# Optimization experiments

Hardware: AMD Instinct MI355X
Metric: run time of the kernel (lower is better)

## Reference

```python
import jax, jax.numpy as jnp
import numpy as np

ROI, P = 28, 7          # ROI window on feature map; output grid 7x7 -> 4x4 bins
BIN = ROI // P
C, CLASSES = 64, 2      # channels after vgg features[:2]; n classes
H = W = 512
N_ROI = 2000
D_FC = 4096


def setup_inputs() -> dict:
    key = jax.random.key(0)
    k = jax.random.split(key, 8)
    s = 0.02
    return {
        "img": jax.random.normal(k[0], (3, H, W), jnp.float32),
        "regions": jax.random.randint(k[1], (N_ROI, 2), 0, H - ROI, jnp.int32),
        "conv_w": jax.random.normal(k[2], (C, 3, 3, 3), jnp.float32) * s,
        "conv_b": jnp.zeros((C,), jnp.float32),
        "fc1_w": jax.random.normal(k[3], (D_FC, C * P * P), jnp.float32) * s,
        "fc1_b": jnp.zeros((D_FC,), jnp.float32),
        "fc2_w": jax.random.normal(k[4], (D_FC, D_FC), jnp.float32) * s,
        "fc2_b": jnp.zeros((D_FC,), jnp.float32),
        "cls_w": jax.random.normal(k[5], (CLASSES, D_FC), jnp.float32) * s,
        "cls_b": jnp.zeros((CLASSES,), jnp.float32),
        "bbox_w": jax.random.normal(k[6], (CLASSES * 4, D_FC), jnp.float32) * s,
        "bbox_b": jnp.zeros((CLASSES * 4,), jnp.float32),
    }


def reference(img, regions, conv_w, conv_b, fc1_w, fc1_b,
              fc2_w, fc2_b, cls_w, cls_b, bbox_w, bbox_b):
    # conv trunk: vgg16.features[:2] = Conv2d(3,64,3,pad=1) + ReLU
    fmap = jax.lax.conv_general_dilated(
        img[None], conv_w, window_strides=(1, 1), padding="SAME",
        dimension_numbers=("NCHW", "OIHW", "NCHW"))[0]
    fmap = jax.nn.relu(fmap + conv_b[:, None, None])        # [C, H, W]

    # per-region crop (irregular gather), vectorized over regions
    def crop(rc):
        return jax.lax.dynamic_slice(fmap, (0, rc[0], rc[1]), (C, ROI, ROI))
    rois = jax.vmap(crop)(regions)                          # [N, C, ROI, ROI]

    # RoI max pooling: divide ROIxROI window into PxP grid, max each bin
    pooled = rois.reshape(N_ROI, C, P, BIN, P, BIN).max(axis=(3, 5))  # [N,C,P,P]
    feat = pooled.reshape(N_ROI, C * P * P)

    # vgg classifier[:-1] (Dropout = identity at inference)
    feat = jax.nn.relu(feat @ fc1_w.T + fc1_b)
    feat = jax.nn.relu(feat @ fc2_w.T + fc2_b)              # [N, 4096]

    cls_logits = feat @ cls_w.T + cls_b                     # [N, CLASSES]
    loc_bbox = feat @ bbox_w.T + bbox_b                     # [N, CLASSES*4]
    return (cls_logits, loc_bbox)
```

## Files before the change

kernel.cpp:

```cpp
#include <hip/hip_runtime.h>

typedef unsigned short u16;
typedef unsigned int u32;
using bf16x8 = __attribute__((ext_vector_type(8))) short;
using f32x4  = __attribute__((ext_vector_type(4))) float;
using ushort8 = __attribute__((ext_vector_type(8))) unsigned short;

__device__ __forceinline__ u16 f2bf(float f) {
  u32 u = __float_as_uint(f);
  return (u16)((u + 0x7FFFu + ((u >> 16) & 1u)) >> 16);
}
__device__ __forceinline__ float bf2f(u16 h) {
  return __uint_as_float(((u32)h) << 16);
}
__device__ __forceinline__ ushort8 umax8(ushort8 a, ushort8 b) {
  return __builtin_elementwise_max(a, b);
}
__device__ __forceinline__ void cvt_chunk(const float* __restrict__ in,
                                          u16* __restrict__ out, int i) {
  float4 v = ((const float4*)in)[i];
  uint2 o;
  o.x = (u32)f2bf(v.x) | ((u32)f2bf(v.y) << 16);
  o.y = (u32)f2bf(v.z) | ((u32)f2bf(v.w) << 16);
  ((uint2*)out)[i] = o;
}

__global__ __launch_bounds__(512) void conv_vmax_k(
    const float* __restrict__ img, const float* __restrict__ w,
    const float* __restrict__ bias, u16* __restrict__ M1,
    const float* __restrict__ w1f, u16* __restrict__ w1b) {
  const int t = threadIdx.x;
  const int bid = blockIdx.x;
  const int r3 = bid % 3, q3 = bid / 3;
  if (r3 == 2) {
    int idx = q3 * 512 + t;
    for (int i = idx; i < 3211264; i += 262144) cvt_chunk(w1f, w1b, i);
    return;
  }
  const int widx = q3 * 2 + r3;
  const int x = ((widx & 15) << 5) + (t >> 4);
  const int cq = (t & 15) << 2;
  const int y0 = (widx >> 4) << 3;

  float wr[27][4];
#pragma unroll
  for (int p = 0; p < 27; ++p)
#pragma unroll
    for (int c = 0; c < 4; ++c) wr[p][c] = w[(cq + c) * 27 + p];
  float bz[4];
#pragma unroll
  for (int c = 0; c < 4; ++c) bz[c] = bias[cq + c];

  const bool xm = (x > 0), xp = (x < 511);
  float win[3][3][3];

#define LOADROW(yy, s)                                                        \
  do {                                                                        \
    if ((yy) >= 0 && (yy) <= 511) {                                          \
      _Pragma("unroll") for (int ci = 0; ci < 3; ++ci) {                      \
        const float* rp = img + ci * 262144 + (yy) * 512 + x;                 \
        win[ci][s][0] = xm ? rp[-1] : 0.f;                                    \
        win[ci][s][1] = rp[0];                                                \
        win[ci][s][2] = xp ? rp[1] : 0.f;                                     \
      }                                                                        \
    } else {                                                                   \
      _Pragma("unroll") for (int ci = 0; ci < 3; ++ci) {                      \
        win[ci][s][0] = 0.f; win[ci][s][1] = 0.f; win[ci][s][2] = 0.f;        \
      }                                                                        \
    }                                                                          \
  } while (0)

  LOADROW(y0 - 1, 0);
  LOADROW(y0, 1);

  float h0[4], h1[4], h2[4], cur[4];
#pragma unroll
  for (int i = 0; i < 11; ++i) {
    const int r = y0 + i;
    LOADROW(r + 1, 2);
    if (r <= 511) {
#pragma unroll
      for (int c = 0; c < 4; ++c) cur[c] = bz[c];
#pragma unroll
      for (int ci = 0; ci < 3; ++ci)
#pragma unroll
        for (int ky = 0; ky < 3; ++ky)
#pragma unroll
          for (int kx = 0; kx < 3; ++kx) {
            const float iv = win[ci][ky][kx];
            const int p = ci * 9 + ky * 3 + kx;
#pragma unroll
            for (int c = 0; c < 4; ++c) cur[c] = fmaf(wr[p][c], iv, cur[c]);
          }
#pragma unroll
      for (int c = 0; c < 4; ++c) cur[c] = fmaxf(cur[c], 0.f);
    } else {
#pragma unroll
      for (int c = 0; c < 4; ++c) cur[c] = 0.f;
    }
    if (i >= 3) {
      const int ym = r - 3;
      float m[4];
#pragma unroll
      for (int c = 0; c < 4; ++c)
        m[c] = fmaxf(fmaxf(h0[c], h1[c]), fmaxf(h2[c], cur[c]));
      uint2 o;
      o.x = (u32)f2bf(m[0]) | ((u32)f2bf(m[1]) << 16);
      o.y = (u32)f2bf(m[2]) | ((u32)f2bf(m[3]) << 16);
      *(uint2*)(M1 + (((size_t)(ym * 512 + x)) << 6) + cq) = o;
    }
#pragma unroll
    for (int c = 0; c < 4; ++c) { h0[c] = h1[c]; h1[c] = h2[c]; h2[c] = cur[c]; }
#pragma unroll
    for (int ci = 0; ci < 3; ++ci)
#pragma unroll
      for (int kx = 0; kx < 3; ++kx) {
        win[ci][0][kx] = win[ci][1][kx];
        win[ci][1][kx] = win[ci][2][kx];
      }
  }
#undef LOADROW
}

__global__ __launch_bounds__(256) void roipool2_k(
    const u16* __restrict__ M1, const int* __restrict__ regions,
    u16* __restrict__ feat, const float* __restrict__ w2f,
    u16* __restrict__ w2b) {
  const int t = threadIdx.x;
  const int bid = blockIdx.x;
  const int r5 = bid % 5, q5 = bid / 5;
  if (r5 == 4) {
    int idx = q5 * 256 + t;
    for (int i = idx; i < 4194304; i += 131072) cvt_chunk(w2f, w2b, i);
    return;
  }
  const int n = q5 * 4 + r5;
  uint4* fdst = (uint4*)(feat + (size_t)n * 3136);
  if (n >= 2000) {
    uint4 z; z.x = z.y = z.z = z.w = 0u;
    for (int w = t; w < 392; w += 256) fdst[w] = z;
    return;
  }
  __shared__ u16 frow[3136];
  int r0 = regions[2 * n], c0 = regions[2 * n + 1];
  for (int w = t; w < 392; w += 256) {
    int bin = w >> 3, cg = w & 7;
    int py = bin / 7, px = bin % 7;
    int y = r0 + py * 4, xb = c0 + px * 4;
    const u16* base = M1 + (((size_t)(y * 512 + xb)) << 6) + cg * 8;
    ushort8 a = *(const ushort8*)(base);
    ushort8 b = *(const ushort8*)(base + 64);
    ushort8 c = *(const ushort8*)(base + 128);
    ushort8 d = *(const ushort8*)(base + 192);
    ushort8 m = umax8(umax8(a, b), umax8(c, d));
#pragma unroll
    for (int k = 0; k < 8; ++k) frow[(cg * 8 + k) * 49 + bin] = m[k];
  }
  __syncthreads();
  const uint4* fsrc = (const uint4*)frow;
  for (int w = t; w < 392; w += 256) fdst[w] = fsrc[w];
}

__global__ __launch_bounds__(512, 2) void gemm_sk_k(
    const u16* __restrict__ A, const u16* __restrict__ B,
    u16* __restrict__ P, int K, int NT0, int NTtot) {
  __shared__ uint4 lds4[6144];
  char* ldsb = (char*)lds4;
  const int t = threadIdx.x;
  const int lane = t & 63, wv = t >> 6;
  const int wm = wv >> 2, wn = wv & 3;

  const int bid = blockIdx.x;
  const int xcd = bid & 7, q = bid >> 3;
  const int sk = xcd >> 2;
  const int mb = q & 7;
  const int nb = ((xcd & 3) << 2) | (q >> 3);
  const int m0 = mb * 256, n0 = nb * 256;
  const int ts = sk ? NT0 : 0;
  const int NTb = sk ? (NTtot - NT0) : NT0;

  const u16* __restrict__ Ab = A + (size_t)m0 * K;
  const u16* __restrict__ Bb = B + (size_t)n0 * K;
  const int srow = t >> 2;
  const int sslot = (t & 3) ^ ((srow >> 1) & 3);
  const u16* pA  = Ab + (size_t)srow * K + sslot * 8;
  const u16* pA2 = pA + (size_t)128 * K;
  const u16* pB  = Bb + (size_t)srow * K + sslot * 8;
  const u16* pB2 = pB + (size_t)128 * K;
  const int dof = t * 16;

#define G2L(src, ldst)                                                        \
  __builtin_amdgcn_global_load_lds(                                          \
      (const __attribute__((address_space(1))) void*)(src),                  \
      (__attribute__((address_space(3))) void*)(ldst), 16, 0, 0)
#define LOFF(r, s) (((r) << 6) + ((((s) ^ (((r) >> 1) & 3))) << 4))

  const int row16 = lane & 15, sl = lane >> 4;
  f32x4 acc[8][4] = {};
  bf16x8 afr[8], bfr[4];

  {
    const size_t k0 = (size_t)ts * 32;
    char* b0 = ldsb;
    G2L(pA + k0, b0 + dof);          G2L(pA2 + k0, b0 + 8192 + dof);
    G2L(pB + k0, b0 + 16384 + dof);  G2L(pB2 + k0, b0 + 24576 + dof);
    if (NTb > 1) {
      char* b1 = ldsb + 32768;
      G2L(pA + k0 + 32, b1 + dof);          G2L(pA2 + k0 + 32, b1 + 8192 + dof);
      G2L(pB + k0 + 32, b1 + 16384 + dof);  G2L(pB2 + k0 + 32, b1 + 24576 + dof);
      asm volatile("s_waitcnt vmcnt(4)" ::: "memory");
    } else {
      asm volatile("s_waitcnt vmcnt(0)" ::: "memory");
    }
  }
  __builtin_amdgcn_s_barrier();

  int cb = 0;
  for (int tt = 0; tt < NTb; ++tt) {
    const int pb = (cb + 2 >= 3) ? cb - 1 : cb + 2;
    const bool pf = (tt + 2) < NTb;
    char* cbuf = ldsb + cb * 32768;
    if (pf) {
      char* fbuf = ldsb + pb * 32768;
      const size_t kof = (size_t)(ts + tt + 2) * 32;
      G2L(pA + kof, fbuf + dof);          G2L(pA2 + kof, fbuf + 8192 + dof);
      G2L(pB + kof, fbuf + 16384 + dof);  G2L(pB2 + kof, fbuf + 24576 + dof);
    }
    __builtin_amdgcn_sched_barrier(0);
    __builtin_amdgcn_s_setprio(1);
    char* Bc = cbuf + 16384;
#pragma unroll
    for (int j = 0; j < 4; ++j)
      bfr[j] = *(const bf16x8*)(Bc + LOFF(wn * 64 + j * 16 + row16, sl));
#pragma unroll
    for (int i = 0; i < 8; ++i)
      afr[i] = *(const bf16x8*)(cbuf + LOFF(wm * 128 + i * 16 + row16, sl));
#pragma unroll
    for (int i = 0; i < 8; ++i)
#pragma unroll
      for (int j = 0; j < 4; ++j)
        acc[i][j] = __builtin_amdgcn_mfma_f32_16x16x32_bf16(afr[i], bfr[j], acc[i][j], 0, 0, 0);
    __builtin_amdgcn_s_setprio(0);
    if (pf) {
      asm volatile("s_waitcnt vmcnt(4)" ::: "memory");
    } else if (tt + 1 < NTb) {
      asm volatile("s_waitcnt vmcnt(0)" ::: "memory");
    }
    __builtin_amdgcn_s_barrier();
    cb = (cb == 2) ? 0 : cb + 1;
  }
#undef G2L
#undef LOFF

  u16* Pb = P + (size_t)sk * 8388608;
#pragma unroll
  for (int i = 0; i < 8; ++i)
#pragma unroll
    for (int j = 0; j < 4; ++j) {
      const int cg = n0 + wn * 64 + j * 16 + row16;
#pragma unroll
      for (int r = 0; r < 4; ++r) {
        const int rg = m0 + wm * 128 + i * 16 + sl * 4 + r;
        Pb[(size_t)rg * 4096 + cg] = f2bf(acc[i][j][r]);
      }
    }
}

__global__ __launch_bounds__(256) void finalize1_k(
    const u16* __restrict__ P, const float* __restrict__ bias,
    u16* __restrict__ H) {
  int c = blockIdx.x * 256 + threadIdx.x;
  int row = c >> 9, c8 = (c & 511) << 3;
  size_t off = (size_t)row * 4096 + c8;
  ushort8 a = *(const ushort8*)(P + off);
  ushort8 b = *(const ushort8*)(P + 8388608 + off);
  float4 b0 = *(const float4*)(bias + c8);
  float4 b1 = *(const float4*)(bias + c8 + 4);
  float v[8];
#pragma unroll
  for (int e = 0; e < 8; ++e) v[e] = bf2f(a[e]) + bf2f(b[e]);
  v[0] += b0.x; v[1] += b0.y; v[2] += b0.z; v[3] += b0.w;
  v[4] += b1.x; v[5] += b1.y; v[6] += b1.z; v[7] += b1.w;
  uint4 o;
  o.x = (u32)f2bf(fmaxf(v[0], 0.f)) | ((u32)f2bf(fmaxf(v[1], 0.f)) << 16);
  o.y = (u32)f2bf(fmaxf(v[2], 0.f)) | ((u32)f2bf(fmaxf(v[3], 0.f)) << 16);
  o.z = (u32)f2bf(fmaxf(v[4], 0.f)) | ((u32)f2bf(fmaxf(v[5], 0.f)) << 16);
  o.w = (u32)f2bf(fmaxf(v[6], 0.f)) | ((u32)f2bf(fmaxf(v[7], 0.f)) << 16);
  *(uint4*)(H + off) = o;
}

__global__ __launch_bounds__(256) void heads2_k(
    const u16* __restrict__ P, const float* __restrict__ bias,
    const float* __restrict__ cw, const float* __restrict__ cb,
    const float* __restrict__ bw, const float* __restrict__ bb,
    float* __restrict__ out) {
  __shared__ u16 wl[10][4096];
  __shared__ float red[4][10];
  const int t = threadIdx.x;
  for (int i4 = t; i4 < 10240; i4 += 256) {
    int j = i4 >> 10, k4 = i4 & 1023;
    float4 v = (j < 2) ? ((const float4*)cw)[j * 1024 + k4]
                       : ((const float4*)bw)[(j - 2) * 1024 + k4];
    uint2 o;
    o.x = (u32)f2bf(v.x) | ((u32)f2bf(v.y) << 16);
    o.y = (u32)f2bf(v.z) | ((u32)f2bf(v.w) << 16);
    *(uint2*)(&wl[j][k4 * 4]) = o;
  }
  __syncthreads();
  const int lane = t & 63, wvi = t >> 6;
  const int m0 = blockIdx.x * 8;
  for (int mi = 0; mi < 8; ++mi) {
    const int m = m0 + mi;
    if (m >= 2000) break;
    const size_t roff = (size_t)m * 4096;
    float p[10];
#pragma unroll
    for (int j = 0; j < 10; ++j) p[j] = 0.f;
#pragma unroll
    for (int h = 0; h < 2; ++h) {
      const int kc = t + h * 256;
      const int c8 = kc * 8;
      ushort8 a = *(const ushort8*)(P + roff + c8);
      ushort8 b2 = *(const ushort8*)(P + 8388608 + roff + c8);
      float4 bi0 = *(const float4*)(bias + c8);
      float4 bi1 = *(const float4*)(bias + c8 + 4);
      float hf[8];
      hf[0] = fmaxf(bf2f(a[0]) + bf2f(b2[0]) + bi0.x, 0.f);
      hf[1] = fmaxf(bf2f(a[1]) + bf2f(b2[1]) + bi0.y, 0.f);
      hf[2] = fmaxf(bf2f(a[2]) + bf2f(b2[2]) + bi0.z, 0.f);
      hf[3] = fmaxf(bf2f(a[3]) + bf2f(b2[3]) + bi0.w, 0.f);
      hf[4] = fmaxf(bf2f(a[4]) + bf2f(b2[4]) + bi1.x, 0.f);
      hf[5] = fmaxf(bf2f(a[5]) + bf2f(b2[5]) + bi1.y, 0.f);
      hf[6] = fmaxf(bf2f(a[6]) + bf2f(b2[6]) + bi1.z, 0.f);
      hf[7] = fmaxf(bf2f(a[7]) + bf2f(b2[7]) + bi1.w, 0.f);
#pragma unroll
      for (int j = 0; j < 10; ++j) {
        ushort8 wv = *(const ushort8*)(&wl[j][c8]);
#pragma unroll
        for (int e = 0; e < 8; ++e) p[j] = fmaf(hf[e], bf2f(wv[e]), p[j]);
      }
    }
#pragma unroll
    for (int j = 0; j < 10; ++j)
#pragma unroll
      for (int off = 32; off > 0; off >>= 1) p[j] += __shfl_down(p[j], off);
    if (lane == 0) {
#pragma unroll
      for (int j = 0; j < 10; ++j) red[wvi][j] = p[j];
    }
    __syncthreads();
    if (t < 10) {
      float s = red[0][t] + red[1][t] + red[2][t] + red[3][t];
      s += (t < 2) ? cb[t] : bb[t - 2];
      if (t < 2) out[m * 2 + t] = s;
      else out[4000 + m * 8 + (t - 2)] = s;
    }
    __syncthreads();
  }
}

extern "C" void kernel_launch(void* const* d_in, const int* in_sizes, int n_in,
                              void* d_out, int out_size, void* d_ws, size_t ws_size,
                              hipStream_t stream) {
  const float* img    = (const float*)d_in[0];
  const int*   regions= (const int*)d_in[1];
  const float* conv_w = (const float*)d_in[2];
  const float* conv_b = (const float*)d_in[3];
  const float* fc1_w  = (const float*)d_in[4];
  const float* fc1_b  = (const float*)d_in[5];
  const float* fc2_w  = (const float*)d_in[6];
  const float* fc2_b  = (const float*)d_in[7];
  const float* cls_w  = (const float*)d_in[8];
  const float* cls_b  = (const float*)d_in[9];
  const float* bbox_w = (const float*)d_in[10];
  const float* bbox_b = (const float*)d_in[11];
  float* out = (float*)d_out;

  char* ws = (char*)d_ws;
  u16* M1   = (u16*)(ws);
  u16* P    = (u16*)(ws);
  u16* feat = (u16*)(ws + 33554432);
  u16* w1b  = (u16*)(ws + 46399488);
  u16* h1   = (u16*)(ws + 46399488);
  u16* w2b  = (u16*)(ws + 72089600);

  conv_vmax_k<<<1536, 512, 0, stream>>>(img, conv_w, conv_b, M1, fc1_w, w1b);
  roipool2_k<<<2560, 256, 0, stream>>>(M1, regions, feat, fc2_w, w2b);
  gemm_sk_k<<<256, 512, 0, stream>>>(feat, w1b, P, 3136, 49, 98);
  finalize1_k<<<4096, 256, 0, stream>>>(P, fc1_b, h1);
  gemm_sk_k<<<256, 512, 0, stream>>>(h1, w2b, P, 4096, 64, 128);
  heads2_k<<<250, 256, 0, stream>>>(P, fc2_b, cls_w, cls_b, bbox_w, bbox_b, out);
}
```

Before: 230.8 us.

## Shrink GEMM block tile to 128x256 with 4 waves and more blocks

The split-K GEMM moves from 256x256 tiles with 8 waves per block to 128x256 tiles with 4 waves per block, launched as 512 blocks instead of 256. The block-to-tile mapping changes from an XCD-aware scheme to a split-K parity bit plus a swizzle over tile indices. The LDS stage buffers shrink to match. The goal is better wave distribution across CUs and higher occupancy, at the cost of less operand reuse per block and more global traffic for B.

```diff
diff --git a/kernel.cpp b/kernel.cpp
--- a/kernel.cpp
+++ b/kernel.cpp
@@ -161,21 +161,20 @@
   for (int w = t; w < 392; w += 256) fdst[w] = fsrc[w];
 }
 
-__global__ __launch_bounds__(512, 2) void gemm_sk_k(
+__global__ __launch_bounds__(256, 2) void gemm_sk4_k(
     const u16* __restrict__ A, const u16* __restrict__ B,
     u16* __restrict__ P, int K, int NT0, int NTtot) {
-  __shared__ uint4 lds4[6144];
+  __shared__ uint4 lds4[4608];
   char* ldsb = (char*)lds4;
   const int t = threadIdx.x;
   const int lane = t & 63, wv = t >> 6;
-  const int wm = wv >> 2, wn = wv & 3;
 
   const int bid = blockIdx.x;
-  const int xcd = bid & 7, q = bid >> 3;
-  const int sk = xcd >> 2;
-  const int mb = q & 7;
-  const int nb = ((xcd & 3) << 2) | (q >> 3);
-  const int m0 = mb * 256, n0 = nb * 256;
+  const int sk = bid & 1;
+  const int q = bid >> 1;
+  const int swz = ((q & 7) << 5) | (q >> 3);
+  const int nb = swz >> 4, mb = swz & 15;
+  const int m0 = mb * 128, n0 = nb * 256;
   const int ts = sk ? NT0 : 0;
   const int NTb = sk ? (NTtot - NT0) : NT0;
 
@@ -183,10 +182,12 @@
   const u16* __restrict__ Bb = B + (size_t)n0 * K;
   const int srow = t >> 2;
   const int sslot = (t & 3) ^ ((srow >> 1) & 3);
-  const u16* pA  = Ab + (size_t)srow * K + sslot * 8;
-  const u16* pA2 = pA + (size_t)128 * K;
-  const u16* pB  = Bb + (size_t)srow * K + sslot * 8;
-  const u16* pB2 = pB + (size_t)128 * K;
+  const u16* pA0 = Ab + (size_t)srow * K + sslot * 8;
+  const u16* pA1 = pA0 + (size_t)64 * K;
+  const u16* pB0 = Bb + (size_t)srow * K + sslot * 8;
+  const u16* pB1 = pB0 + (size_t)64 * K;
+  const u16* pB2 = pB0 + (size_t)128 * K;
+  const u16* pB3 = pB0 + (size_t)192 * K;
   const int dof = t * 16;
 
 #define G2L(src, ldst)                                                        \
@@ -194,6 +195,15 @@
       (const __attribute__((address_space(1))) void*)(src),                  \
       (__attribute__((address_space(3))) void*)(ldst), 16, 0, 0)
 #define LOFF(r, s) (((r) << 6) + ((((s) ^ (((r) >> 1) & 3))) << 4))
+#define STAGE6(koff, buf)                                                     \
+  do {                                                                        \
+    G2L(pA0 + (koff), (buf) + dof);                                           \
+    G2L(pA1 + (koff), (buf) + 4096 + dof);                                    \
+    G2L(pB0 + (koff), (buf) + 8192 + dof);                                    \
+    G2L(pB1 + (koff), (buf) + 12288 + dof);                                   \
+    G2L(pB2 + (koff), (buf) + 16384 + dof);                                   \
+    G2L(pB3 + (koff), (buf) + 20480 + dof);                                   \
+  } while (0)
 
   const int row16 = lane & 15, sl = lane >> 4;
   f32x4 acc[8][4] = {};
@@ -201,14 +211,10 @@
 
   {
     const size_t k0 = (size_t)ts * 32;
-    char* b0 = ldsb;
-    G2L(pA + k0, b0 + dof);          G2L(pA2 + k0, b0 + 8192 + dof);
-    G2L(pB + k0, b0 + 16384 + dof);  G2L(pB2 + k0, b0 + 24576 + dof);
+    STAGE6(k0, ldsb);
     if (NTb > 1) {
-      char* b1 = ldsb + 32768;
-      G2L(pA + k0 + 32, b1 + dof);          G2L(pA2 + k0 + 32, b1 + 8192 + dof);
-      G2L(pB + k0 + 32, b1 + 16384 + dof);  G2L(pB2 + k0 + 32, b1 + 24576 + dof);
-      asm volatile("s_waitcnt vmcnt(4)" ::: "memory");
+      STAGE6(k0 + 32, ldsb + 24576);
+      asm volatile("s_waitcnt vmcnt(6)" ::: "memory");
     } else {
       asm volatile("s_waitcnt vmcnt(0)" ::: "memory");
     }
@@ -219,22 +225,20 @@
   for (int tt = 0; tt < NTb; ++tt) {
     const int pb = (cb + 2 >= 3) ? cb - 1 : cb + 2;
     const bool pf = (tt + 2) < NTb;
-    char* cbuf = ldsb + cb * 32768;
+    char* cbuf = ldsb + cb * 24576;
     if (pf) {
-      char* fbuf = ldsb + pb * 32768;
-      const size_t kof = (size_t)(ts + tt + 2) * 32;
-      G2L(pA + kof, fbuf + dof);          G2L(pA2 + kof, fbuf + 8192 + dof);
-      G2L(pB + kof, fbuf + 16384 + dof);  G2L(pB2 + kof, fbuf + 24576 + dof);
+      char* fbuf = ldsb + pb * 24576;
+      STAGE6((size_t)(ts + tt + 2) * 32, fbuf);
     }
     __builtin_amdgcn_sched_barrier(0);
     __builtin_amdgcn_s_setprio(1);
-    char* Bc = cbuf + 16384;
+    char* Bc = cbuf + 8192;
 #pragma unroll
     for (int j = 0; j < 4; ++j)
-      bfr[j] = *(const bf16x8*)(Bc + LOFF(wn * 64 + j * 16 + row16, sl));
+      bfr[j] = *(const bf16x8*)(Bc + LOFF(wv * 64 + j * 16 + row16, sl));
 #pragma unroll
     for (int i = 0; i < 8; ++i)
-      afr[i] = *(const bf16x8*)(cbuf + LOFF(wm * 128 + i * 16 + row16, sl));
+      afr[i] = *(const bf16x8*)(cbuf + LOFF(i * 16 + row16, sl));
 #pragma unroll
     for (int i = 0; i < 8; ++i)
 #pragma unroll
@@ -242,13 +246,14 @@
         acc[i][j] = __builtin_amdgcn_mfma_f32_16x16x32_bf16(afr[i], bfr[j], acc[i][j], 0, 0, 0);
     __builtin_amdgcn_s_setprio(0);
     if (pf) {
-      asm volatile("s_waitcnt vmcnt(4)" ::: "memory");
+      asm volatile("s_waitcnt vmcnt(6)" ::: "memory");
     } else if (tt + 1 < NTb) {
       asm volatile("s_waitcnt vmcnt(0)" ::: "memory");
     }
     __builtin_amdgcn_s_barrier();
     cb = (cb == 2) ? 0 : cb + 1;
   }
+#undef STAGE6
 #undef G2L
 #undef LOFF
 
@@ -257,10 +262,10 @@
   for (int i = 0; i < 8; ++i)
 #pragma unroll
     for (int j = 0; j < 4; ++j) {
-      const int cg = n0 + wn * 64 + j * 16 + row16;
+      const int cg = n0 + wv * 64 + j * 16 + row16;
 #pragma unroll
       for (int r = 0; r < 4; ++r) {
-        const int rg = m0 + wm * 128 + i * 16 + sl * 4 + r;
+        const int rg = m0 + i * 16 + sl * 4 + r;
         Pb[(size_t)rg * 4096 + cg] = f2bf(acc[i][j][r]);
       }
     }
@@ -335,9 +340,9 @@
       hf[7] = fmaxf(bf2f(a[7]) + bf2f(b2[7]) + bi1.w, 0.f);
 #pragma unroll
       for (int j = 0; j < 10; ++j) {
-        ushort8 wv = *(const ushort8*)(&wl[j][c8]);
-#pragma unroll
-        for (int e = 0; e < 8; ++e) p[j] = fmaf(hf[e], bf2f(wv[e]), p[j]);
+        ushort8 wvv = *(const ushort8*)(&wl[j][c8]);
+#pragma unroll
+        for (int e = 0; e < 8; ++e) p[j] = fmaf(hf[e], bf2f(wvv[e]), p[j]);
       }
     }
 #pragma unroll
@@ -386,8 +391,8 @@
 
   conv_vmax_k<<<1536, 512, 0, stream>>>(img, conv_w, conv_b, M1, fc1_w, w1b);
   roipool2_k<<<2560, 256, 0, stream>>>(M1, regions, feat, fc2_w, w2b);
-  gemm_sk_k<<<256, 512, 0, stream>>>(feat, w1b, P, 3136, 49, 98);
+  gemm_sk4_k<<<512, 256, 0, stream>>>(feat, w1b, P, 3136, 49, 98);
   finalize1_k<<<4096, 256, 0, stream>>>(P, fc1_b, h1);
-  gemm_sk_k<<<256, 512, 0, stream>>>(h1, w2b, P, 4096, 64, 128);
+  gemm_sk4_k<<<512, 256, 0, stream>>>(h1, w2b, P, 4096, 64, 128);
   heads2_k<<<250, 256, 0, stream>>>(P, fc2_b, cls_w, cls_b, bbox_w, bbox_b, out);
 }
```

New measurement: 238.7 us (median of 2 runs). 3.4% more time.
